# Kernel tuning notes

Hardware: AMD Instinct MI355X
Metric: run time of the kernel (lower is better)

The kernel has to match this reference:

```python
import jax, jax.numpy as jnp
import numpy as np

NEG = -9e9  # large negative used by the original torch code for masking


def setup_inputs() -> dict:
    key = jax.random.key(0)
    k1, k2, k3, k4 = jax.random.split(key, 4)
    B, N, L, D = 64, 128, 64, 768
    return {
        "text_embeddings": jax.random.normal(k1, (B, N, D), dtype=jnp.float32),
        "image_embeddings": jax.random.normal(k2, (B, L, D), dtype=jnp.float32),
        "text_mask": jax.random.randint(k3, (B, N), 0, 2, dtype=jnp.int32),
        "image_mask": jax.random.randint(k4, (B, L), 0, 2, dtype=jnp.int32),
    }


def _grounding(text_emb, image_emb, text_mask, image_mask):
    # Vectorized version of the B x B python loop in score_grounding.
    tm = text_mask.astype(text_emb.dtype)   # [B, N]
    im = image_mask.astype(text_emb.dtype)  # [B, L]
    # pairwise mask: mask[i, j, n, l] = text_mask[i, n] * image_mask[j, l]
    mask = tm[:, None, :, None] * im[None, :, None, :]            # [B, B, N, L]
    att = jnp.einsum('ind,jld->ijnl', text_emb, image_emb) * mask  # [B, B, N, L]
    att = jnp.where(att * mask != 0, att, NEG)
    # softmax over image spans (last dim), masked
    aw_first = jax.nn.softmax(att, axis=-1) * mask
    score1 = (aw_first * att).sum(-1).mean(-1)                     # [B, B]
    # softmax over text spans (dim 2 == the N axis), masked (transpose trick in torch)
    aw_second = jax.nn.softmax(att, axis=2) * mask
    score2 = (aw_second * att).sum(-1).mean(-1)                    # [B, B]
    sent_scores = score1 + score2                                  # [B, B]
    B = text_emb.shape[0]
    idx = jnp.arange(B)
    token_scores = att[idx, idx]                                   # diagonal pairs, [B, N, L]
    return sent_scores, token_scores


def reference(text_embeddings, image_embeddings, text_mask, image_mask):
    B = text_embeddings.shape[0]
    S, token_scores = _grounding(text_embeddings, image_embeddings, text_mask, image_mask)
    # text_emb_i2s = softmax(att_weights) @ image_emb
    text_emb_i2s = jnp.einsum('bnl,bld->bnd', jax.nn.softmax(token_scores, axis=-1), image_embeddings)
    # loss = -(sum diag logsoftmax(S, dim=1) + sum diag logsoftmax(S.T, dim=1)) / n
    ls1 = jnp.diagonal(jax.nn.log_softmax(S, axis=1))
    ls2 = jnp.diagonal(jax.nn.log_softmax(S.T, axis=1))
    loss = -(jnp.sum(ls1) + jnp.sum(ls2)) / B
    return loss, text_emb_i2s
```

## Files before the change

kernel.cpp:

```cpp
#include <hip/hip_runtime.h>
#include <math.h>

#define BSZ 64
#define NN  128
#define LL  64
#define DD  768
#define NEGV (-9e9f)

#define TQ (BSZ * NN * DD / 4)
#define IQ (BSZ * LL * DD / 4)

typedef _Float16 f16x8 __attribute__((ext_vector_type(8)));
typedef __attribute__((ext_vector_type(4))) float f32x4;

__device__ __forceinline__ void gl_lds16(const void* g, void* l) {
    __builtin_amdgcn_global_load_lds(
        (const __attribute__((address_space(1))) void*)g,
        (__attribute__((address_space(3))) void*)l, 16, 0, 0);
}

__global__ __launch_bounds__(256) void k_prep(
    const float4* __restrict__ t4, const float4* __restrict__ g4,
    ushort4* __restrict__ A, ushort4* __restrict__ B)
{
    int id = blockIdx.x * 256 + threadIdx.x;
    const float4* src; ushort4* dst; int idx;
    if (id < TQ) { src = t4; dst = A; idx = id; }
    else         { src = g4; dst = B; idx = id - TQ; }
    float4 x = src[idx];
    _Float16 h0 = (_Float16)x.x, h1 = (_Float16)x.y;
    _Float16 h2 = (_Float16)x.z, h3 = (_Float16)x.w;
    ushort4 o;
    o.x = __builtin_bit_cast(unsigned short, h0);
    o.y = __builtin_bit_cast(unsigned short, h1);
    o.z = __builtin_bit_cast(unsigned short, h2);
    o.w = __builtin_bit_cast(unsigned short, h3);
    dst[idx] = o;
}

__device__ __forceinline__ void stage_chunk(
    const unsigned short* __restrict__ pa, const unsigned short* __restrict__ pb,
    int k0, char* buf, int wave, int lane)
{
    int rsub = lane >> 3;
    int k8s  = lane & 7;
#pragma unroll
    for (int c = 0; c < 4; c++) {
        int r  = c * 32 + wave * 8 + rsub;
        int k8 = k8s ^ (r & 7);
        gl_lds16(pa + (size_t)r * DD + k0 + k8 * 8, buf + c * 4096 + wave * 1024);
        gl_lds16(pb + (size_t)r * DD + k0 + k8 * 8, buf + 16384 + c * 4096 + wave * 1024);
    }
}

__global__ __launch_bounds__(256, 2) void k_scores(
    const unsigned short* __restrict__ A, const unsigned short* __restrict__ B,
    const int* __restrict__ tmask, const int* __restrict__ imask,
    float* __restrict__ S, float* __restrict__ W)
{
    union SmemU {
        char  stage[2][32768];
        float Cs[NN][129];
    };
    __shared__ SmemU u;
    __shared__ float tmi[NN];
    __shared__ float imj[NN];
    __shared__ float rowred[256];
    __shared__ float colred[NN];

    const int bid = blockIdx.x;
    const int grp = bid >> 4, idx = bid & 15;
    const int i  = (grp >> 3) * 4 + (idx >> 2);
    const int jj = (grp & 7) * 4 + (idx & 3);
    const int j0 = jj * 2;

    const int tid  = threadIdx.x;
    const int wave = tid >> 6;
    const int lane = tid & 63;
    const int quad = lane >> 4;
    const int l15  = lane & 15;
    const int rh   = wave & 1;
    const int ch   = wave >> 1;

    if (tid < NN) {
        tmi[tid] = tmask[i * NN + tid] ? 1.f : 0.f;
        imj[tid] = imask[j0 * LL + tid] ? 1.f : 0.f;
    }

    const unsigned short* pa = A + (size_t)i * NN * DD;
    const unsigned short* pb = B + (size_t)j0 * LL * DD;

    f32x4 acc[4][4];
    const f32x4 zf = {0.f, 0.f, 0.f, 0.f};
#pragma unroll
    for (int tr = 0; tr < 4; tr++)
#pragma unroll
        for (int tc = 0; tc < 4; tc++) acc[tr][tc] = zf;

    stage_chunk(pa, pb, 0, u.stage[0], wave, lane);
    __syncthreads();

    for (int c = 0; c < 12; c++) {
        if (c + 1 < 12)
            stage_chunk(pa, pb, (c + 1) << 6, u.stage[(c + 1) & 1], wave, lane);
        const char* Ab = u.stage[c & 1];
        const char* Bb = Ab + 16384;
#pragma unroll
        for (int s = 0; s < 2; s++) {
            int k8q = s * 4 + quad;
            int sw  = k8q ^ (l15 & 7);
            f16x8 af[4], bfr[4];
#pragma unroll
            for (int t = 0; t < 4; t++) {
                int row = rh * 64 + t * 16 + l15;
                af[t]  = *(const f16x8*)(Ab + ((row << 3) + sw) * 16);
                int col = ch * 64 + t * 16 + l15;
                bfr[t] = *(const f16x8*)(Bb + ((col << 3) + sw) * 16);
            }
#pragma unroll
            for (int tr = 0; tr < 4; tr++)
#pragma unroll
                for (int tc = 0; tc < 4; tc++)
                    acc[tr][tc] = __builtin_amdgcn_mfma_f32_16x16x32_f16(
                        af[tr], bfr[tc], acc[tr][tc], 0, 0, 0);
        }
        __syncthreads();
    }

#pragma unroll
    for (int tr = 0; tr < 4; tr++) {
        int rb = rh * 64 + tr * 16 + quad * 4;
#pragma unroll
        for (int tc = 0; tc < 4; tc++) {
            int col = ch * 64 + tc * 16 + l15;
            float im = imj[col];
#pragma unroll
            for (int rr = 0; rr < 4; rr++) {
                int row = rb + rr;
                float v = acc[tr][tc][rr];
                bool keep = (tmi[row] != 0.f) && (im != 0.f) && (v != 0.f);
                u.Cs[row][col] = keep ? v : NEGV;
            }
        }
    }
    __syncthreads();

    {
        int jh = tid >> 7, n = tid & 127;
        const float* Crow = &u.Cs[n][jh * 64];
        float m = -INFINITY;
        for (int l = 0; l < LL; l++) m = fmaxf(m, Crow[l]);
        float ssum = 0.f, ws = 0.f;
        for (int l = 0; l < LL; l++) {
            float v = Crow[l];
            float e = __expf(v - m);
            ssum += e;
            ws += imj[jh * 64 + l] * e * v;
        }
        rowred[tid] = tmi[n] * (ws / ssum);
    }
    __syncthreads();

    if (tid < NN) {
        int jh = tid >> 6, l = tid & 63;
        float m = -INFINITY;
        for (int n = 0; n < NN; n++) m = fmaxf(m, u.Cs[n][jh * 64 + l]);
        float ssum = 0.f, ws = 0.f;
        for (int n = 0; n < NN; n++) {
            float v = u.Cs[n][jh * 64 + l];
            float e = __expf(v - m);
            ssum += e;
            ws += tmi[n] * e * v;
        }
        colred[tid] = imj[jh * 64 + l] * (ws / ssum);
    } else if (jj == (i >> 1)) {
        int jh = i & 1;
        int n = tid & 127;
        const float* Crow = &u.Cs[n][jh * 64];
        float m = -INFINITY;
        for (int l = 0; l < LL; l++) m = fmaxf(m, Crow[l]);
        float ssum = 0.f;
        for (int l = 0; l < LL; l++) ssum += __expf(Crow[l] - m);
        float inv = 1.f / ssum;
        float* Wb = W + (size_t)i * LL * NN;
        for (int l = 0; l < LL; l++)
            Wb[(size_t)l * NN + n] = __expf(Crow[l] - m) * inv;
    }
    __syncthreads();

    if (tid < NN) {
        int jh = tid >> 6, t = tid & 63;
        float p = rowred[jh * 128 + t] + rowred[jh * 128 + 64 + t] + colred[jh * 64 + t];
#pragma unroll
        for (int off = 32; off; off >>= 1) p += __shfl_down(p, off);
        if (t == 0) S[i * BSZ + j0 + jh] = p / (float)NN;
    }
}

__global__ __launch_bounds__(256) void k_i2s(
    const float* __restrict__ W, const float* __restrict__ img,
    float* __restrict__ out)
{
    __shared__ float Ws[LL][16];
    const int b  = blockIdx.x;
    const int ng = blockIdx.z * 16;
    const int d  = blockIdx.y * 256 + threadIdx.x;
    const float* Wb = W + (size_t)b * LL * NN;

    {
        int t4 = threadIdx.x * 4;
        int l = t4 >> 4, noff = t4 & 15;
        float4 w = *(const float4*)(Wb + (size_t)l * NN + ng + noff);
        Ws[l][noff + 0] = w.x; Ws[l][noff + 1] = w.y;
        Ws[l][noff + 2] = w.z; Ws[l][noff + 3] = w.w;
    }
    __syncthreads();

    const float* ib = img + (size_t)b * LL * DD;
    float* ob = out + 1 + (size_t)b * NN * DD + (size_t)ng * DD;

    float acc[16];
#pragma unroll
    for (int q = 0; q < 16; q++) acc[q] = 0.f;
    for (int l = 0; l < LL; l++) {
        float g = ib[(size_t)l * DD + d];
#pragma unroll
        for (int q = 0; q < 16; q++)
            acc[q] = fmaf(Ws[l][q], g, acc[q]);
    }
#pragma unroll
    for (int q = 0; q < 16; q++)
        ob[(size_t)q * DD + d] = acc[q];
}

__global__ void k_loss(const float* __restrict__ S, float* __restrict__ out)
{
    const int t = threadIdx.x;
    float diag = S[t * BSZ + t];
    float m1 = -INFINITY, m2 = -INFINITY;
    for (int jj = 0; jj < BSZ; jj++) {
        m1 = fmaxf(m1, S[t * BSZ + jj]);
        m2 = fmaxf(m2, S[jj * BSZ + t]);
    }
    float s1 = 0.f, s2 = 0.f;
    for (int jj = 0; jj < BSZ; jj++) {
        s1 += __expf(S[t * BSZ + jj] - m1);
        s2 += __expf(S[jj * BSZ + t] - m2);
    }
    float p = 2.f * diag - (m1 + logf(s1)) - (m2 + logf(s2));
#pragma unroll
    for (int off = 32; off; off >>= 1) p += __shfl_down(p, off);
    if (t == 0) out[0] = -p / (float)BSZ;
}

extern "C" void kernel_launch(void* const* d_in, const int* in_sizes, int n_in,
                              void* d_out, int out_size, void* d_ws, size_t ws_size,
                              hipStream_t stream)
{
    (void)in_sizes; (void)n_in; (void)out_size; (void)ws_size;
    const float* text = (const float*)d_in[0];
    const float* img  = (const float*)d_in[1];
    const int*   tm   = (const int*)d_in[2];
    const int*   im   = (const int*)d_in[3];
    float* out = (float*)d_out;

    char* ws = (char*)d_ws;
    unsigned short* A = (unsigned short*)(ws);
    unsigned short* B = (unsigned short*)(ws + 12582912);
    float* S = (float*)(ws + 18874368);
    float* W = (float*)(ws + 18890752);

    k_prep<<<(TQ + IQ) / 256, 256, 0, stream>>>(
        (const float4*)text, (const float4*)img, (ushort4*)A, (ushort4*)B);

    k_scores<<<BSZ * (BSZ / 2), 256, 0, stream>>>(A, B, tm, im, S, W);

    dim3 g2(BSZ, 3, 8);
    k_i2s<<<g2, 256, 0, stream>>>(W, img, out);

    k_loss<<<1, 64, 0, stream>>>(S, out);
}
```

Baseline: 186.1 us.

## Enlarge score tiles to 256x256, do softmax reductions in registers, restructure i2s

The scores kernel now uses 512-thread blocks covering two text batches times four image batches (a 256x256 tile), which cuts redundant global-to-LDS staging of A and B. The LDS C-matrix spill is gone: row and column softmax statistics are computed directly from MFMA accumulators using cross-lane shuffles and small shared partial buffers, and the diagonal weights W are written from registers. k_i2s now loads the whole W block into LDS once and loops over all n-groups per block, and k_loss stages S in shared memory. The larger register footprint (32 accumulator tiles per thread) risks lower occupancy, and the grid shrinks to 512 blocks.

Result: slower. 211.6 us (+13.7%).

```diff
diff --git a/kernel.cpp b/kernel.cpp
--- a/kernel.cpp
+++ b/kernel.cpp
@@ -46,154 +46,199 @@
     int k8s  = lane & 7;
 #pragma unroll
     for (int c = 0; c < 4; c++) {
-        int r  = c * 32 + wave * 8 + rsub;
+        int r  = c * 64 + wave * 8 + rsub;
         int k8 = k8s ^ (r & 7);
-        gl_lds16(pa + (size_t)r * DD + k0 + k8 * 8, buf + c * 4096 + wave * 1024);
-        gl_lds16(pb + (size_t)r * DD + k0 + k8 * 8, buf + 16384 + c * 4096 + wave * 1024);
-    }
-}
-
-__global__ __launch_bounds__(256, 2) void k_scores(
+        gl_lds16(pa + (size_t)r * DD + k0 + k8 * 8, buf + c * 8192 + wave * 1024);
+        gl_lds16(pb + (size_t)r * DD + k0 + k8 * 8, buf + 32768 + c * 8192 + wave * 1024);
+    }
+}
+
+__global__ __launch_bounds__(512, 2) void k_scores(
     const unsigned short* __restrict__ A, const unsigned short* __restrict__ B,
     const int* __restrict__ tmask, const int* __restrict__ imask,
     float* __restrict__ S, float* __restrict__ W)
 {
-    union SmemU {
-        char  stage[2][32768];
-        float Cs[NN][129];
-    };
-    __shared__ SmemU u;
-    __shared__ float tmi[NN];
-    __shared__ float imj[NN];
-    __shared__ float rowred[256];
-    __shared__ float colred[NN];
+    __shared__ __align__(16) char stage[2][65536];
+    __shared__ float tmi[256];
+    __shared__ float imj[256];
+    __shared__ float rowredL[256][4];
+    __shared__ float cpmax[4][256];
+    __shared__ float cpes[4][256];
+    __shared__ float cpws[4][256];
 
     const int bid = blockIdx.x;
     const int grp = bid >> 4, idx = bid & 15;
-    const int i  = (grp >> 3) * 4 + (idx >> 2);
-    const int jj = (grp & 7) * 4 + (idx & 3);
-    const int j0 = jj * 2;
+    const int ip = (grp >> 2) * 4 + (idx >> 2);
+    const int jq = (grp & 3) * 4 + (idx & 3);
 
     const int tid  = threadIdx.x;
     const int wave = tid >> 6;
     const int lane = tid & 63;
     const int quad = lane >> 4;
     const int l15  = lane & 15;
-    const int rh   = wave & 1;
-    const int ch   = wave >> 1;
-
-    if (tid < NN) {
-        tmi[tid] = tmask[i * NN + tid] ? 1.f : 0.f;
-        imj[tid] = imask[j0 * LL + tid] ? 1.f : 0.f;
-    }
-
-    const unsigned short* pa = A + (size_t)i * NN * DD;
-    const unsigned short* pb = B + (size_t)j0 * LL * DD;
-
-    f32x4 acc[4][4];
+    const int wr   = wave & 3;
+    const int wc   = wave >> 2;
+    const int ih   = wr >> 1;
+
+    if (tid < 256) tmi[tid] = tmask[ip * 256 + tid] ? 1.f : 0.f;
+    else           imj[tid - 256] = imask[jq * 256 + (tid - 256)] ? 1.f : 0.f;
+
+    const unsigned short* pa = A + (size_t)ip * 2 * NN * DD;
+    const unsigned short* pb = B + (size_t)jq * 4 * LL * DD;
+
+    f32x4 acc[4][8];
     const f32x4 zf = {0.f, 0.f, 0.f, 0.f};
 #pragma unroll
     for (int tr = 0; tr < 4; tr++)
 #pragma unroll
-        for (int tc = 0; tc < 4; tc++) acc[tr][tc] = zf;
-
-    stage_chunk(pa, pb, 0, u.stage[0], wave, lane);
+        for (int tc = 0; tc < 8; tc++) acc[tr][tc] = zf;
+
+    stage_chunk(pa, pb, 0, stage[0], wave, lane);
     __syncthreads();
 
     for (int c = 0; c < 12; c++) {
         if (c + 1 < 12)
-            stage_chunk(pa, pb, (c + 1) << 6, u.stage[(c + 1) & 1], wave, lane);
-        const char* Ab = u.stage[c & 1];
-        const char* Bb = Ab + 16384;
+            stage_chunk(pa, pb, (c + 1) << 6, stage[(c + 1) & 1], wave, lane);
+        const char* Ab = stage[c & 1];
+        const char* Bb = Ab + 32768;
 #pragma unroll
         for (int s = 0; s < 2; s++) {
-            int k8q = s * 4 + quad;
-            int sw  = k8q ^ (l15 & 7);
-            f16x8 af[4], bfr[4];
-#pragma unroll
-            for (int t = 0; t < 4; t++) {
-                int row = rh * 64 + t * 16 + l15;
-                af[t]  = *(const f16x8*)(Ab + ((row << 3) + sw) * 16);
-                int col = ch * 64 + t * 16 + l15;
-                bfr[t] = *(const f16x8*)(Bb + ((col << 3) + sw) * 16);
+            int sw = (((s * 4 + quad) ^ (l15 & 7)) << 4);
+            f16x8 af[4], bfr[8];
+#pragma unroll
+            for (int tr = 0; tr < 4; tr++) {
+                int row = wr * 64 + tr * 16 + l15;
+                af[tr] = *(const f16x8*)(Ab + (row << 7) + sw);
+            }
+#pragma unroll
+            for (int tc = 0; tc < 8; tc++) {
+                int col = wc * 128 + tc * 16 + l15;
+                bfr[tc] = *(const f16x8*)(Bb + (col << 7) + sw);
             }
 #pragma unroll
             for (int tr = 0; tr < 4; tr++)
 #pragma unroll
-                for (int tc = 0; tc < 4; tc++)
+                for (int tc = 0; tc < 8; tc++)
                     acc[tr][tc] = __builtin_amdgcn_mfma_f32_16x16x32_f16(
                         af[tr], bfr[tc], acc[tr][tc], 0, 0, 0);
         }
         __syncthreads();
     }
 
+    float tmr[4][4];
+    float imc[8];
+#pragma unroll
+    for (int tr = 0; tr < 4; tr++)
+#pragma unroll
+        for (int rr = 0; rr < 4; rr++)
+            tmr[tr][rr] = tmi[wr * 64 + tr * 16 + quad * 4 + rr];
+#pragma unroll
+    for (int tc = 0; tc < 8; tc++)
+        imc[tc] = imj[wc * 128 + tc * 16 + l15];
+
+    const bool isdiag = (jq == (ip >> 1));
+    const int  jneed  = ip * 2 + ih - jq * 4;
+
 #pragma unroll
     for (int tr = 0; tr < 4; tr++) {
-        int rb = rh * 64 + tr * 16 + quad * 4;
-#pragma unroll
-        for (int tc = 0; tc < 4; tc++) {
-            int col = ch * 64 + tc * 16 + l15;
-            float im = imj[col];
+#pragma unroll
+        for (int rr = 0; rr < 4; rr++) {
+            int row = wr * 64 + tr * 16 + quad * 4 + rr;
+            float tm = tmr[tr][rr];
+#pragma unroll
+            for (int jl = 0; jl < 2; jl++) {
+                float vmv[4];
+                float m = -INFINITY;
+#pragma unroll
+                for (int t = 0; t < 4; t++) {
+                    int tc = jl * 4 + t;
+                    float v = acc[tr][tc][rr];
+                    float vm = (tm != 0.f && imc[tc] != 0.f && v != 0.f) ? v : NEGV;
+                    vmv[t] = vm;
+                    m = fmaxf(m, vm);
+                }
+                m = fmaxf(m, __shfl_xor(m, 1));
+                m = fmaxf(m, __shfl_xor(m, 2));
+                m = fmaxf(m, __shfl_xor(m, 4));
+                m = fmaxf(m, __shfl_xor(m, 8));
+                float ss = 0.f, ws = 0.f;
+#pragma unroll
+                for (int t = 0; t < 4; t++) {
+                    float e = __expf(vmv[t] - m);
+                    ss += e;
+                    ws += imc[jl * 4 + t] * e * vmv[t];
+                }
+                ss += __shfl_xor(ss, 1); ss += __shfl_xor(ss, 2);
+                ss += __shfl_xor(ss, 4); ss += __shfl_xor(ss, 8);
+                ws += __shfl_xor(ws, 1); ws += __shfl_xor(ws, 2);
+                ws += __shfl_xor(ws, 4); ws += __shfl_xor(ws, 8);
+                if (l15 == 0) rowredL[row][wc * 2 + jl] = tm * (ws / ss);
+                if (isdiag && (wc * 2 + jl) == jneed) {
+                    float inv = 1.f / ss;
+                    float* Wb = W + (size_t)(ip * 2 + ih) * LL * NN;
+                    int n = row & 127;
+#pragma unroll
+                    for (int t = 0; t < 4; t++) {
+                        float e = __expf(vmv[t] - m) * inv;
+                        Wb[(size_t)(t * 16 + l15) * NN + n] = e;
+                    }
+                }
+            }
+        }
+    }
+
+#pragma unroll
+    for (int tc = 0; tc < 8; tc++) {
+        int col = wc * 128 + tc * 16 + l15;
+        float cm = -INFINITY;
+#pragma unroll
+        for (int tr = 0; tr < 4; tr++)
 #pragma unroll
             for (int rr = 0; rr < 4; rr++) {
-                int row = rb + rr;
                 float v = acc[tr][tc][rr];
-                bool keep = (tmi[row] != 0.f) && (im != 0.f) && (v != 0.f);
-                u.Cs[row][col] = keep ? v : NEGV;
-            }
-        }
+                float vm = (tmr[tr][rr] != 0.f && imc[tc] != 0.f && v != 0.f) ? v : NEGV;
+                cm = fmaxf(cm, vm);
+            }
+        cm = fmaxf(cm, __shfl_xor(cm, 16));
+        cm = fmaxf(cm, __shfl_xor(cm, 32));
+        if (quad == 0) cpmax[wr][col] = cm;
+    }
+    __syncthreads();
+
+#pragma unroll
+    for (int tc = 0; tc < 8; tc++) {
+        int col = wc * 128 + tc * 16 + l15;
+        float m2 = fmaxf(cpmax[ih * 2][col], cpmax[ih * 2 + 1][col]);
+        float es = 0.f, ws = 0.f;
+#pragma unroll
+        for (int tr = 0; tr < 4; tr++)
+#pragma unroll
+            for (int rr = 0; rr < 4; rr++) {
+                float v = acc[tr][tc][rr];
+                float tm = tmr[tr][rr];
+                float vm = (tm != 0.f && imc[tc] != 0.f && v != 0.f) ? v : NEGV;
+                float e = __expf(vm - m2);
+                es += e;
+                ws += tm * e * vm;
+            }
+        es += __shfl_xor(es, 16); es += __shfl_xor(es, 32);
+        ws += __shfl_xor(ws, 16); ws += __shfl_xor(ws, 32);
+        if (quad == 0) { cpes[wr][col] = es; cpws[wr][col] = ws; }
     }
     __syncthreads();
 
     {
-        int jh = tid >> 7, n = tid & 127;
-        const float* Crow = &u.Cs[n][jh * 64];
-        float m = -INFINITY;
-        for (int l = 0; l < LL; l++) m = fmaxf(m, Crow[l]);
-        float ssum = 0.f, ws = 0.f;
-        for (int l = 0; l < LL; l++) {
-            float v = Crow[l];
-            float e = __expf(v - m);
-            ssum += e;
-            ws += imj[jh * 64 + l] * e * v;
-        }
-        rowred[tid] = tmi[n] * (ws / ssum);
-    }
-    __syncthreads();
-
-    if (tid < NN) {
-        int jh = tid >> 6, l = tid & 63;
-        float m = -INFINITY;
-        for (int n = 0; n < NN; n++) m = fmaxf(m, u.Cs[n][jh * 64 + l]);
-        float ssum = 0.f, ws = 0.f;
-        for (int n = 0; n < NN; n++) {
-            float v = u.Cs[n][jh * 64 + l];
-            float e = __expf(v - m);
-            ssum += e;
-            ws += tmi[n] * e * v;
-        }
-        colred[tid] = imj[jh * 64 + l] * (ws / ssum);
-    } else if (jj == (i >> 1)) {
-        int jh = i & 1;
-        int n = tid & 127;
-        const float* Crow = &u.Cs[n][jh * 64];
-        float m = -INFINITY;
-        for (int l = 0; l < LL; l++) m = fmaxf(m, Crow[l]);
-        float ssum = 0.f;
-        for (int l = 0; l < LL; l++) ssum += __expf(Crow[l] - m);
-        float inv = 1.f / ssum;
-        float* Wb = W + (size_t)i * LL * NN;
-        for (int l = 0; l < LL; l++)
-            Wb[(size_t)l * NN + n] = __expf(Crow[l] - m) * inv;
-    }
-    __syncthreads();
-
-    if (tid < NN) {
-        int jh = tid >> 6, t = tid & 63;
-        float p = rowred[jh * 128 + t] + rowred[jh * 128 + 64 + t] + colred[jh * 64 + t];
+        int aih = wave >> 2, jloc = wave & 3;
+        float p = rowredL[aih * 128 + lane][jloc]
+                + rowredL[aih * 128 + 64 + lane][jloc];
+        int col = jloc * 64 + lane;
+        float es = cpes[aih * 2][col] + cpes[aih * 2 + 1][col];
+        float ws = cpws[aih * 2][col] + cpws[aih * 2 + 1][col];
+        p += imj[col] * (ws / es);
 #pragma unroll
         for (int off = 32; off; off >>= 1) p += __shfl_down(p, off);
-        if (t == 0) S[i * BSZ + j0 + jh] = p / (float)NN;
+        if (lane == 0)
+            S[(ip * 2 + aih) * BSZ + jq * 4 + jloc] = p * (1.f / 128.f);
     }
 }
 
@@ -201,56 +246,71 @@
     const float* __restrict__ W, const float* __restrict__ img,
     float* __restrict__ out)
 {
-    __shared__ float Ws[LL][16];
-    const int b  = blockIdx.x;
-    const int ng = blockIdx.z * 16;
-    const int d  = blockIdx.y * 256 + threadIdx.x;
+    __shared__ float Ws[LL * NN];
+    const int b = blockIdx.x, tid = threadIdx.x;
     const float* Wb = W + (size_t)b * LL * NN;
-
-    {
-        int t4 = threadIdx.x * 4;
-        int l = t4 >> 4, noff = t4 & 15;
-        float4 w = *(const float4*)(Wb + (size_t)l * NN + ng + noff);
-        Ws[l][noff + 0] = w.x; Ws[l][noff + 1] = w.y;
-        Ws[l][noff + 2] = w.z; Ws[l][noff + 3] = w.w;
-    }
-    __syncthreads();
-
-    const float* ib = img + (size_t)b * LL * DD;
-    float* ob = out + 1 + (size_t)b * NN * DD + (size_t)ng * DD;
-
-    float acc[16];
-#pragma unroll
-    for (int q = 0; q < 16; q++) acc[q] = 0.f;
-    for (int l = 0; l < LL; l++) {
-        float g = ib[(size_t)l * DD + d];
+#pragma unroll
+    for (int q = 0; q < 8; q++) {
+        int o = (tid + q * 256) * 4;
+        *(float4*)&Ws[o] = *(const float4*)&Wb[o];
+    }
+    __syncthreads();
+
+    const int d = blockIdx.y * 256 + tid;
+    const float* ib = img + (size_t)b * LL * DD + d;
+    float* ob = out + 1 + (size_t)b * NN * DD + d;
+
+    for (int ng = 0; ng < 8; ng++) {
+        float acc[16];
+#pragma unroll
+        for (int q = 0; q < 16; q++) acc[q] = 0.f;
+        for (int l = 0; l < LL; l++) {
+            float g = ib[(size_t)l * DD];
+            const float* wrow = &Ws[l * NN + ng * 16];
+            float4 w0 = *(const float4*)(wrow);
+            float4 w1 = *(const float4*)(wrow + 4);
+            float4 w2 = *(const float4*)(wrow + 8);
+            float4 w3 = *(const float4*)(wrow + 12);
+            acc[0]  = fmaf(w0.x, g, acc[0]);  acc[1]  = fmaf(w0.y, g, acc[1]);
+            acc[2]  = fmaf(w0.z, g, acc[2]);  acc[3]  = fmaf(w0.w, g, acc[3]);
+            acc[4]  = fmaf(w1.x, g, acc[4]);  acc[5]  = fmaf(w1.y, g, acc[5]);
+            acc[6]  = fmaf(w1.z, g, acc[6]);  acc[7]  = fmaf(w1.w, g, acc[7]);
+            acc[8]  = fmaf(w2.x, g, acc[8]);  acc[9]  = fmaf(w2.y, g, acc[9]);
+            acc[10] = fmaf(w2.z, g, acc[10]); acc[11] = fmaf(w2.w, g, acc[11]);
+            acc[12] = fmaf(w3.x, g, acc[12]); acc[13] = fmaf(w3.y, g, acc[13]);
+            acc[14] = fmaf(w3.z, g, acc[14]); acc[15] = fmaf(w3.w, g, acc[15]);
+        }
 #pragma unroll
         for (int q = 0; q < 16; q++)
-            acc[q] = fmaf(Ws[l][q], g, acc[q]);
-    }
-#pragma unroll
-    for (int q = 0; q < 16; q++)
-        ob[(size_t)q * DD + d] = acc[q];
-}
-
-__global__ void k_loss(const float* __restrict__ S, float* __restrict__ out)
-{
-    const int t = threadIdx.x;
-    float diag = S[t * BSZ + t];
-    float m1 = -INFINITY, m2 = -INFINITY;
-    for (int jj = 0; jj < BSZ; jj++) {
-        m1 = fmaxf(m1, S[t * BSZ + jj]);
-        m2 = fmaxf(m2, S[jj * BSZ + t]);
-    }
-    float s1 = 0.f, s2 = 0.f;
-    for (int jj = 0; jj < BSZ; jj++) {
-        s1 += __expf(S[t * BSZ + jj] - m1);
-        s2 += __expf(S[jj * BSZ + t] - m2);
-    }
-    float p = 2.f * diag - (m1 + logf(s1)) - (m2 + logf(s2));
-#pragma unroll
-    for (int off = 32; off; off >>= 1) p += __shfl_down(p, off);
-    if (t == 0) out[0] = -p / (float)BSZ;
+            ob[(size_t)(ng * 16 + q) * DD] = acc[q];
+    }
+}
+
+__global__ __launch_bounds__(256) void k_loss(
+    const float* __restrict__ S, float* __restrict__ out)
+{
+    __shared__ float Ss[BSZ * BSZ];
+    const int tid = threadIdx.x;
+#pragma unroll
+    for (int q = 0; q < 16; q++) Ss[tid + q * 256] = S[tid + q * 256];
+    __syncthreads();
+    if (tid < 64) {
+        float diag = Ss[tid * BSZ + tid];
+        float m1 = -INFINITY, m2 = -INFINITY;
+        for (int jj = 0; jj < BSZ; jj++) {
+            m1 = fmaxf(m1, Ss[tid * BSZ + jj]);
+            m2 = fmaxf(m2, Ss[jj * BSZ + tid]);
+        }
+        float s1 = 0.f, s2 = 0.f;
+        for (int jj = 0; jj < BSZ; jj++) {
+            s1 += __expf(Ss[tid * BSZ + jj] - m1);
+            s2 += __expf(Ss[jj * BSZ + tid] - m2);
+        }
+        float p = 2.f * diag - (m1 + logf(s1)) - (m2 + logf(s2));
+#pragma unroll
+        for (int off = 32; off; off >>= 1) p += __shfl_down(p, off);
+        if (tid == 0) out[0] = -p / (float)BSZ;
+    }
 }
 
 extern "C" void kernel_launch(void* const* d_in, const int* in_sizes, int n_in,
@@ -273,10 +333,10 @@
     k_prep<<<(TQ + IQ) / 256, 256, 0, stream>>>(
         (const float4*)text, (const float4*)img, (ushort4*)A, (ushort4*)B);
 
-    k_scores<<<BSZ * (BSZ / 2), 256, 0, stream>>>(A, B, tm, im, S, W);
-
-    dim3 g2(BSZ, 3, 8);
+    k_scores<<<512, 512, 0, stream>>>(A, B, tm, im, S, W);
+
+    dim3 g2(BSZ, 3);
     k_i2s<<<g2, 256, 0, stream>>>(W, img, out);
 
-    k_loss<<<1, 64, 0, stream>>>(S, out);
-}
+    k_loss<<<1, 256, 0, stream>>>(S, out);
+}
```
